# Kernel tuning notes

Measured on AMD Instinct MI355X. Metric: run time of the kernel, lower is better.

The kernel has to match this reference:

```python
import jax, jax.numpy as jnp
import numpy as np

K = 4
REG_MAX = 32


def setup_inputs() -> dict:
    key = jax.random.key(0)
    ks = jax.random.split(key, 6)
    B, L, C = 8, 100000, 80
    scores = jax.random.normal(ks[0], (B, L, C), dtype=jnp.float32)
    pred_corners = jax.random.normal(ks[1], (B, L, 4 * (REG_MAX + 1)), dtype=jnp.float32)
    in_dim = 4 * (K + 1)  # 20
    hidden = 64
    w1 = jax.random.normal(ks[2], (in_dim, hidden), dtype=jnp.float32) * (1.0 / np.sqrt(in_dim))
    b1 = jax.random.normal(ks[3], (hidden,), dtype=jnp.float32) * 0.01
    w2 = jax.random.normal(ks[4], (hidden, 1), dtype=jnp.float32) * (1.0 / np.sqrt(hidden))
    b2 = jax.random.normal(ks[5], (1,), dtype=jnp.float32) * 0.01
    return {"scores": scores, "pred_corners": pred_corners,
            "w1": w1, "b1": b1, "w2": w2, "b2": b2}


def reference(scores, pred_corners, w1, b1, w2, b2):
    B, L, _ = pred_corners.shape
    # [B, L, 4, reg_max+1]
    prob = jax.nn.softmax(pred_corners.reshape(B, L, 4, REG_MAX + 1), axis=-1)
    topk, _ = jax.lax.top_k(prob, K)                       # [B, L, 4, k]
    stat = jnp.concatenate([topk, topk.mean(-1, keepdims=True)], axis=-1)  # [B, L, 4, k+1]
    stat = stat.reshape(B, L, 4 * (K + 1))                 # [B, L, 20]
    h = jax.nn.silu(stat @ w1 + b1)                        # [B, L, 64]
    quality = h @ w2 + b2                                  # [B, L, 1]
    return scores + quality
```

## Files before the change

kernel.cpp:

```cpp
#include <hip/hip_runtime.h>

#define LOG2E 1.4426950408889634f

typedef __attribute__((address_space(3))) unsigned int lds_u32_t;
typedef const __attribute__((address_space(1))) unsigned int glb_u32_t;
typedef __fp16 h2 __attribute__((ext_vector_type(2)));
typedef __fp16 h8 __attribute__((ext_vector_type(8)));

__global__ __launch_bounds__(256) void lqe_wave6(
    const float* __restrict__ scores,
    const float* __restrict__ pred,
    const float* __restrict__ w1,
    const float* __restrict__ b1,
    const float* __restrict__ w2,
    const float* __restrict__ b2,
    float* __restrict__ out)
{
    __shared__ __align__(16) float predS[4 * 2112];
    __shared__ __align__(16) h2    wH[640];
    __shared__ __align__(16) float wSf[132];

    const int t    = threadIdx.x;
    const int lane = t & 63;
    const int wv   = t >> 6;
    const int tile = blockIdx.x;

    for (int e = t; e < 640; e += 256) {
        const int p = e >> 6, h = e & 63;
        float a = w1[p * 128 + h];
        float b = w1[p * 128 + 64 + h];
        wH[e] = __builtin_amdgcn_cvt_pkrtz(a, b);
    }
    if (t < 64) { wSf[t] = b1[t]; wSf[64 + t] = w2[t]; }
    if (t == 0) wSf[128] = b2[0];
    __syncthreads();

    const float* gp  = pred + (size_t)tile * 8448 + wv * 2112;
    float*       buf = predS + wv * 2112;
#pragma unroll
    for (int k = 0; k < 8; ++k) {
        __builtin_amdgcn_global_load_lds((glb_u32_t*)(gp + 256 * k + 4 * lane),
                                         (lds_u32_t*)(buf + 256 * k), 16, 0, 0);
    }
    __builtin_amdgcn_global_load_lds((glb_u32_t*)(gp + 2048 + lane),
                                     (lds_u32_t*)(buf + 2048), 4, 0, 0);

    asm volatile("s_waitcnt vmcnt(0)" ::: "memory");
    __builtin_amdgcn_sched_barrier(0);

    const size_t s4 = (size_t)tile * 1280 + wv * 320;
    const float4* sp = reinterpret_cast<const float4*>(scores) + s4;
    float4 sv0 = sp[lane +   0];
    float4 sv1 = sp[lane +  64];
    float4 sv2 = sp[lane + 128];
    float4 sv3 = sp[lane + 192];
    float4 sv4 = sp[lane + 256];

    const int r = lane >> 2, c = lane & 3;
    const float* xp = buf + r * 132 + c * 33;
    float xs[33];
#pragma unroll
    for (int j = 0; j < 33; ++j) xs[j] = xp[j];

    float t0 = -1e30f, t1 = -1e30f, t2 = -1e30f, t3 = -1e30f;
#pragma unroll
    for (int j = 0; j < 33; ++j) {
        float v  = xs[j];
        float r0 = fminf(t0, v);  t0 = fmaxf(t0, v);
        float r1 = fminf(t1, r0); t1 = fmaxf(t1, r0);
        float r2 = fminf(t2, r1); t2 = fmaxf(t2, r1);
        t3 = fmaxf(t3, r2);
    }
    float denom = 0.f;
#pragma unroll
    for (int j = 0; j < 33; ++j)
        denom += __builtin_amdgcn_exp2f((xs[j] - t0) * LOG2E);
    float rd = __builtin_amdgcn_rcpf(denom);

    float s5[5];
    s5[0] = rd;
    s5[1] = __builtin_amdgcn_exp2f((t1 - t0) * LOG2E) * rd;
    s5[2] = __builtin_amdgcn_exp2f((t2 - t0) * LOG2E) * rd;
    s5[3] = __builtin_amdgcn_exp2f((t3 - t0) * LOG2E) * rd;
    s5[4] = (s5[0] + s5[1] + s5[2] + s5[3]) * 0.25f;

    float stat[20];
#pragma unroll
    for (int i = 0; i < 20; ++i)
        stat[i] = __shfl(s5[i % 5], i / 5, 4);

    h2 spk[10];
#pragma unroll
    for (int p = 0; p < 10; ++p)
        spk[p] = __builtin_amdgcn_cvt_pkrtz(stat[2 * p], stat[2 * p + 1]);

    float hacc[16];
    {
        const float4* b1v = reinterpret_cast<const float4*>(wSf + 16 * c);
#pragma unroll
        for (int k = 0; k < 4; ++k) {
            float4 b = b1v[k];
            hacc[4*k+0]=b.x; hacc[4*k+1]=b.y; hacc[4*k+2]=b.z; hacc[4*k+3]=b.w;
        }
    }
#pragma unroll
    for (int p = 0; p < 10; ++p) {
        const h8* wp = reinterpret_cast<const h8*>(wH + p * 64 + 16 * c);
#pragma unroll
        for (int k = 0; k < 4; ++k) {
            h8 w8 = wp[k];
#pragma unroll
            for (int e = 0; e < 4; ++e) {
                h2 w; w[0] = w8[2*e]; w[1] = w8[2*e+1];
#if __has_builtin(__builtin_amdgcn_fdot2)
                hacc[4*k+e] = __builtin_amdgcn_fdot2(spk[p], w, hacc[4*k+e], false);
#else
                hacc[4*k+e] = fmaf((float)spk[p][0], (float)w[0],
                              fmaf((float)spk[p][1], (float)w[1], hacc[4*k+e]));
#endif
            }
        }
    }

    float q = 0.f;
    {
        const float4* w2v = reinterpret_cast<const float4*>(wSf + 64 + 16 * c);
#pragma unroll
        for (int k = 0; k < 4; ++k) {
            float4 w = w2v[k];
#pragma unroll
            for (int e = 0; e < 4; ++e) {
                float v  = hacc[4*k+e];
                float sg = __builtin_amdgcn_rcpf(1.f + __builtin_amdgcn_exp2f(-v * LOG2E));
                float we = (e == 0) ? w.x : (e == 1) ? w.y : (e == 2) ? w.z : w.w;
                q = fmaf(v * sg, we, q);
            }
        }
    }
    q += __shfl_xor(q, 1, 4);
    q += __shfl_xor(q, 2, 4);
    q += wSf[128];

    float4* op = reinterpret_cast<float4*>(out) + s4;
    {
        float qq; int idx, rl;
        idx = lane +   0; rl = idx / 20; qq = __shfl(q, rl * 4, 64);
        sv0.x+=qq; sv0.y+=qq; sv0.z+=qq; sv0.w+=qq; op[idx] = sv0;
        idx = lane +  64; rl = idx / 20; qq = __shfl(q, rl * 4, 64);
        sv1.x+=qq; sv1.y+=qq; sv1.z+=qq; sv1.w+=qq; op[idx] = sv1;
        idx = lane + 128; rl = idx / 20; qq = __shfl(q, rl * 4, 64);
        sv2.x+=qq; sv2.y+=qq; sv2.z+=qq; sv2.w+=qq; op[idx] = sv2;
        idx = lane + 192; rl = idx / 20; qq = __shfl(q, rl * 4, 64);
        sv3.x+=qq; sv3.y+=qq; sv3.z+=qq; sv3.w+=qq; op[idx] = sv3;
        idx = lane + 256; rl = idx / 20; qq = __shfl(q, rl * 4, 64);
        sv4.x+=qq; sv4.y+=qq; sv4.z+=qq; sv4.w+=qq; op[idx] = sv4;
    }
}

extern "C" void kernel_launch(void* const* d_in, const int* in_sizes, int n_in,
                              void* d_out, int out_size, void* d_ws, size_t ws_size,
                              hipStream_t stream) {
    const float* scores = (const float*)d_in[0];
    const float* pred   = (const float*)d_in[1];
    const float* w1     = (const float*)d_in[2];
    const float* b1     = (const float*)d_in[3];
    const float* w2     = (const float*)d_in[4];
    const float* b2     = (const float*)d_in[5];
    float* out = (float*)d_out;

    const int nrows = in_sizes[1] / 132;
    const int grid  = nrows / 64;

    hipLaunchKernelGGL(lqe_wave6, dim3(grid), dim3(256), 0, stream,
                       scores, pred, w1, b1, w2, b2, out);
}
```

Baseline: 170.2 us.

## Make kernel persistent with grid-stride tiles and overlap scores loads

Converts the one-tile-per-block kernel into a persistent kernel with a fixed grid of 1024 blocks that loop over tiles. This amortizes the per-block weight staging and lets the scores loads overlap the softmax/MLP compute, since the wait is relaxed to vmcnt(5) until just before the stores. Pred loads use a cache-policy flag, output stores become nontemporal, and launch bounds ask for 4 blocks per CU. The risk is lower parallelism per CU from the fixed grid. Also, the LDS buffer is reused across iterations without a barrier, which depends on per-wave private buffers and in-order waits being safe.

Result: faster. 144.3 us (-15.2%).

```diff
diff --git a/kernel.cpp b/kernel.cpp
--- a/kernel.cpp
+++ b/kernel.cpp
@@ -6,15 +6,17 @@
 typedef const __attribute__((address_space(1))) unsigned int glb_u32_t;
 typedef __fp16 h2 __attribute__((ext_vector_type(2)));
 typedef __fp16 h8 __attribute__((ext_vector_type(8)));
+typedef float  f4 __attribute__((ext_vector_type(4)));
 
-__global__ __launch_bounds__(256) void lqe_wave6(
+__global__ __launch_bounds__(256, 4) void lqe_pers(
     const float* __restrict__ scores,
     const float* __restrict__ pred,
     const float* __restrict__ w1,
     const float* __restrict__ b1,
     const float* __restrict__ w2,
     const float* __restrict__ b2,
-    float* __restrict__ out)
+    float* __restrict__ out,
+    int ntiles)
 {
     __shared__ __align__(16) float predS[4 * 2112];
     __shared__ __align__(16) h2    wH[640];
@@ -23,7 +25,6 @@
     const int t    = threadIdx.x;
     const int lane = t & 63;
     const int wv   = t >> 6;
-    const int tile = blockIdx.x;
 
     for (int e = t; e < 640; e += 256) {
         const int p = e >> 6, h = e & 63;
@@ -35,125 +36,130 @@
     if (t == 0) wSf[128] = b2[0];
     __syncthreads();
 
-    const float* gp  = pred + (size_t)tile * 8448 + wv * 2112;
-    float*       buf = predS + wv * 2112;
+    float* buf = predS + wv * 2112;
+
+    for (int tile = blockIdx.x; tile < ntiles; tile += gridDim.x) {
+        const float* gp = pred + (size_t)tile * 8448 + wv * 2112;
 #pragma unroll
-    for (int k = 0; k < 8; ++k) {
-        __builtin_amdgcn_global_load_lds((glb_u32_t*)(gp + 256 * k + 4 * lane),
-                                         (lds_u32_t*)(buf + 256 * k), 16, 0, 0);
-    }
-    __builtin_amdgcn_global_load_lds((glb_u32_t*)(gp + 2048 + lane),
-                                     (lds_u32_t*)(buf + 2048), 4, 0, 0);
+        for (int k = 0; k < 8; ++k) {
+            __builtin_amdgcn_global_load_lds((glb_u32_t*)(gp + 256 * k + 4 * lane),
+                                             (lds_u32_t*)(buf + 256 * k), 16, 0, 2);
+        }
+        __builtin_amdgcn_global_load_lds((glb_u32_t*)(gp + 2048 + lane),
+                                         (lds_u32_t*)(buf + 2048), 4, 0, 2);
 
-    asm volatile("s_waitcnt vmcnt(0)" ::: "memory");
-    __builtin_amdgcn_sched_barrier(0);
+        const size_t s4 = (size_t)tile * 1280 + wv * 320;
+        const f4* sp = reinterpret_cast<const f4*>(scores) + s4;
+        f4 sv0 = sp[lane +   0];
+        f4 sv1 = sp[lane +  64];
+        f4 sv2 = sp[lane + 128];
+        f4 sv3 = sp[lane + 192];
+        f4 sv4 = sp[lane + 256];
 
-    const size_t s4 = (size_t)tile * 1280 + wv * 320;
-    const float4* sp = reinterpret_cast<const float4*>(scores) + s4;
-    float4 sv0 = sp[lane +   0];
-    float4 sv1 = sp[lane +  64];
-    float4 sv2 = sp[lane + 128];
-    float4 sv3 = sp[lane + 192];
-    float4 sv4 = sp[lane + 256];
+        asm volatile("s_waitcnt vmcnt(5)" ::: "memory");
+        __builtin_amdgcn_sched_barrier(0);
 
-    const int r = lane >> 2, c = lane & 3;
-    const float* xp = buf + r * 132 + c * 33;
-    float xs[33];
+        const int r = lane >> 2, c = lane & 3;
+        const float* xp = buf + r * 132 + c * 33;
+        float xs[33];
 #pragma unroll
-    for (int j = 0; j < 33; ++j) xs[j] = xp[j];
+        for (int j = 0; j < 33; ++j) xs[j] = xp[j];
 
-    float t0 = -1e30f, t1 = -1e30f, t2 = -1e30f, t3 = -1e30f;
+        float t0 = -1e30f, t1 = -1e30f, t2 = -1e30f, t3 = -1e30f;
 #pragma unroll
-    for (int j = 0; j < 33; ++j) {
-        float v  = xs[j];
-        float r0 = fminf(t0, v);  t0 = fmaxf(t0, v);
-        float r1 = fminf(t1, r0); t1 = fmaxf(t1, r0);
-        float r2 = fminf(t2, r1); t2 = fmaxf(t2, r1);
-        t3 = fmaxf(t3, r2);
-    }
-    float denom = 0.f;
+        for (int j = 0; j < 33; ++j) {
+            float v  = xs[j];
+            float r0 = fminf(t0, v);  t0 = fmaxf(t0, v);
+            float r1 = fminf(t1, r0); t1 = fmaxf(t1, r0);
+            float r2 = fminf(t2, r1); t2 = fmaxf(t2, r1);
+            t3 = fmaxf(t3, r2);
+        }
+        float denom = 0.f;
 #pragma unroll
-    for (int j = 0; j < 33; ++j)
-        denom += __builtin_amdgcn_exp2f((xs[j] - t0) * LOG2E);
-    float rd = __builtin_amdgcn_rcpf(denom);
+        for (int j = 0; j < 33; ++j)
+            denom += __builtin_amdgcn_exp2f((xs[j] - t0) * LOG2E);
+        float rd = __builtin_amdgcn_rcpf(denom);
 
-    float s5[5];
-    s5[0] = rd;
-    s5[1] = __builtin_amdgcn_exp2f((t1 - t0) * LOG2E) * rd;
-    s5[2] = __builtin_amdgcn_exp2f((t2 - t0) * LOG2E) * rd;
-    s5[3] = __builtin_amdgcn_exp2f((t3 - t0) * LOG2E) * rd;
-    s5[4] = (s5[0] + s5[1] + s5[2] + s5[3]) * 0.25f;
+        float s5[5];
+        s5[0] = rd;
+        s5[1] = __builtin_amdgcn_exp2f((t1 - t0) * LOG2E) * rd;
+        s5[2] = __builtin_amdgcn_exp2f((t2 - t0) * LOG2E) * rd;
+        s5[3] = __builtin_amdgcn_exp2f((t3 - t0) * LOG2E) * rd;
+        s5[4] = (s5[0] + s5[1] + s5[2] + s5[3]) * 0.25f;
 
-    float stat[20];
+        float stat[20];
 #pragma unroll
-    for (int i = 0; i < 20; ++i)
-        stat[i] = __shfl(s5[i % 5], i / 5, 4);
+        for (int i = 0; i < 20; ++i)
+            stat[i] = __shfl(s5[i % 5], i / 5, 4);
 
-    h2 spk[10];
+        h2 spk[10];
 #pragma unroll
-    for (int p = 0; p < 10; ++p)
-        spk[p] = __builtin_amdgcn_cvt_pkrtz(stat[2 * p], stat[2 * p + 1]);
+        for (int p = 0; p < 10; ++p)
+            spk[p] = __builtin_amdgcn_cvt_pkrtz(stat[2 * p], stat[2 * p + 1]);
 
-    float hacc[16];
-    {
-        const float4* b1v = reinterpret_cast<const float4*>(wSf + 16 * c);
+        float hacc[16];
+        {
+            const f4* b1v = reinterpret_cast<const f4*>(wSf + 16 * c);
 #pragma unroll
-        for (int k = 0; k < 4; ++k) {
-            float4 b = b1v[k];
-            hacc[4*k+0]=b.x; hacc[4*k+1]=b.y; hacc[4*k+2]=b.z; hacc[4*k+3]=b.w;
-        }
-    }
-#pragma unroll
-    for (int p = 0; p < 10; ++p) {
-        const h8* wp = reinterpret_cast<const h8*>(wH + p * 64 + 16 * c);
-#pragma unroll
-        for (int k = 0; k < 4; ++k) {
-            h8 w8 = wp[k];
-#pragma unroll
-            for (int e = 0; e < 4; ++e) {
-                h2 w; w[0] = w8[2*e]; w[1] = w8[2*e+1];
-#if __has_builtin(__builtin_amdgcn_fdot2)
-                hacc[4*k+e] = __builtin_amdgcn_fdot2(spk[p], w, hacc[4*k+e], false);
-#else
-                hacc[4*k+e] = fmaf((float)spk[p][0], (float)w[0],
-                              fmaf((float)spk[p][1], (float)w[1], hacc[4*k+e]));
-#endif
+            for (int k = 0; k < 4; ++k) {
+                f4 b = b1v[k];
+                hacc[4*k+0]=b.x; hacc[4*k+1]=b.y; hacc[4*k+2]=b.z; hacc[4*k+3]=b.w;
             }
         }
-    }
-
-    float q = 0.f;
-    {
-        const float4* w2v = reinterpret_cast<const float4*>(wSf + 64 + 16 * c);
 #pragma unroll
-        for (int k = 0; k < 4; ++k) {
-            float4 w = w2v[k];
+        for (int p = 0; p < 10; ++p) {
+            const h8* wp = reinterpret_cast<const h8*>(wH + p * 64 + 16 * c);
 #pragma unroll
-            for (int e = 0; e < 4; ++e) {
-                float v  = hacc[4*k+e];
-                float sg = __builtin_amdgcn_rcpf(1.f + __builtin_amdgcn_exp2f(-v * LOG2E));
-                float we = (e == 0) ? w.x : (e == 1) ? w.y : (e == 2) ? w.z : w.w;
-                q = fmaf(v * sg, we, q);
+            for (int k = 0; k < 4; ++k) {
+                h8 w8 = wp[k];
+#pragma unroll
+                for (int e = 0; e < 4; ++e) {
+                    h2 w; w[0] = w8[2*e]; w[1] = w8[2*e+1];
+#if __has_builtin(__builtin_amdgcn_fdot2)
+                    hacc[4*k+e] = __builtin_amdgcn_fdot2(spk[p], w, hacc[4*k+e], false);
+#else
+                    hacc[4*k+e] = fmaf((float)spk[p][0], (float)w[0],
+                                  fmaf((float)spk[p][1], (float)w[1], hacc[4*k+e]));
+#endif
+                }
             }
         }
-    }
-    q += __shfl_xor(q, 1, 4);
-    q += __shfl_xor(q, 2, 4);
-    q += wSf[128];
 
-    float4* op = reinterpret_cast<float4*>(out) + s4;
-    {
-        float qq; int idx, rl;
-        idx = lane +   0; rl = idx / 20; qq = __shfl(q, rl * 4, 64);
-        sv0.x+=qq; sv0.y+=qq; sv0.z+=qq; sv0.w+=qq; op[idx] = sv0;
-        idx = lane +  64; rl = idx / 20; qq = __shfl(q, rl * 4, 64);
-        sv1.x+=qq; sv1.y+=qq; sv1.z+=qq; sv1.w+=qq; op[idx] = sv1;
-        idx = lane + 128; rl = idx / 20; qq = __shfl(q, rl * 4, 64);
-        sv2.x+=qq; sv2.y+=qq; sv2.z+=qq; sv2.w+=qq; op[idx] = sv2;
-        idx = lane + 192; rl = idx / 20; qq = __shfl(q, rl * 4, 64);
-        sv3.x+=qq; sv3.y+=qq; sv3.z+=qq; sv3.w+=qq; op[idx] = sv3;
-        idx = lane + 256; rl = idx / 20; qq = __shfl(q, rl * 4, 64);
-        sv4.x+=qq; sv4.y+=qq; sv4.z+=qq; sv4.w+=qq; op[idx] = sv4;
+        float q = 0.f;
+        {
+            const f4* w2v = reinterpret_cast<const f4*>(wSf + 64 + 16 * c);
+#pragma unroll
+            for (int k = 0; k < 4; ++k) {
+                f4 w = w2v[k];
+#pragma unroll
+                for (int e = 0; e < 4; ++e) {
+                    float v  = hacc[4*k+e];
+                    float sg = __builtin_amdgcn_rcpf(1.f + __builtin_amdgcn_exp2f(-v * LOG2E));
+                    float we = w[e];
+                    q = fmaf(v * sg, we, q);
+                }
+            }
+        }
+        q += __shfl_xor(q, 1, 4);
+        q += __shfl_xor(q, 2, 4);
+        q += wSf[128];
+
+        asm volatile("s_waitcnt vmcnt(0)" ::: "memory");
+
+        f4* op = reinterpret_cast<f4*>(out) + s4;
+        {
+            float qq; int idx, rl;
+            idx = lane +   0; rl = idx / 20; qq = __shfl(q, rl * 4, 64);
+            sv0 += qq; __builtin_nontemporal_store(sv0, &op[idx]);
+            idx = lane +  64; rl = idx / 20; qq = __shfl(q, rl * 4, 64);
+            sv1 += qq; __builtin_nontemporal_store(sv1, &op[idx]);
+            idx = lane + 128; rl = idx / 20; qq = __shfl(q, rl * 4, 64);
+            sv2 += qq; __builtin_nontemporal_store(sv2, &op[idx]);
+            idx = lane + 192; rl = idx / 20; qq = __shfl(q, rl * 4, 64);
+            sv3 += qq; __builtin_nontemporal_store(sv3, &op[idx]);
+            idx = lane + 256; rl = idx / 20; qq = __shfl(q, rl * 4, 64);
+            sv4 += qq; __builtin_nontemporal_store(sv4, &op[idx]);
+        }
     }
 }
 
@@ -168,9 +174,10 @@
     const float* b2     = (const float*)d_in[5];
     float* out = (float*)d_out;
 
-    const int nrows = in_sizes[1] / 132;
-    const int grid  = nrows / 64;
+    const int nrows  = in_sizes[1] / 132;
+    const int ntiles = nrows / 64;
+    const int grid   = 1024;
 
-    hipLaunchKernelGGL(lqe_wave6, dim3(grid), dim3(256), 0, stream,
-                       scores, pred, w1, b1, w2, b2, out);
+    hipLaunchKernelGGL(lqe_pers, dim3(grid), dim3(256), 0, stream,
+                       scores, pred, w1, b1, w2, b2, out, ntiles);
 }
```
